# Kernel optimization log

Hardware: AMD Instinct MI355X
Metric: run time of the kernel (lower is better)

Reference implementation:

```python
import jax, jax.numpy as jnp
import numpy as np

N_PEGS = 32      # 33 holes, one empty at start
N_ACTIONS = 132  # 33 positions * 4 moves


def _constants():
    # English peg-solitaire board: 7x7 cross, 33 holes; hole 0 is the center (3,3).
    moves = np.array([[-1, 0], [1, 0], [0, -1], [0, 1]], dtype=np.int64)
    cells = [(i, j) for i in range(7) for j in range(7) if (2 <= i <= 4) or (2 <= j <= 4)]
    cells.remove((3, 3))
    grid = np.array([(3, 3)] + cells, dtype=np.int64)          # (33, 2)
    p2i = {tuple(p): k for k, p in enumerate(grid)}
    pos_ids = np.repeat(np.arange(33), 4)                      # (132,)
    move_ids = np.tile(np.arange(4), 33)                       # (132,)
    apos = grid[pos_ids]                                       # (132, 2)
    amov = moves[move_ids]
    midp = apos + amov
    tgtp = apos + 2 * amov
    mid_idx = np.array([p2i.get(tuple(p), 0) for p in midp], dtype=np.int64)
    tgt_idx = np.array([p2i.get(tuple(p), 0) for p in tgtp], dtype=np.int64)
    oob = np.array([(tuple(m) not in p2i) or (tuple(t) not in p2i)
                    for m, t in zip(midp, tgtp)], dtype=bool)  # (132,)
    return dict(
        action_pos_ids=jnp.asarray(pos_ids, dtype=jnp.int32),
        action_mid_indices=jnp.asarray(mid_idx, dtype=jnp.int32),
        action_target_indices=jnp.asarray(tgt_idx, dtype=jnp.int32),
        oob_mask=jnp.asarray(oob),
        i_indices=jnp.asarray(grid[:, 0], dtype=jnp.int32),
        j_indices=jnp.asarray(grid[:, 1], dtype=jnp.int32),
    )


def setup_inputs() -> dict:
    key = jax.random.key(0)
    n = 262144
    k1, k2, k3, k4 = jax.random.split(key, 4)
    pegs = (jax.random.uniform(k1, (n, 33)) > 0.5).astype(jnp.float32)
    n_pegs = jax.random.randint(k2, (n,), 2, 32).astype(jnp.int32)
    done = jnp.zeros((n,), dtype=bool)
    total_reward = jax.random.uniform(k3, (n,), dtype=jnp.float32)
    actions = jax.random.randint(k4, (n,), 0, N_ACTIONS).astype(jnp.int32)
    inp = {"pegs": pegs, "n_pegs": n_pegs, "done": done,
           "total_reward": total_reward, "actions": actions}
    inp.update(_constants())
    return inp


def _feasible(pegs, done, action_pos_ids, action_mid_indices,
              action_target_indices, oob_mask):
    # (n, 132) boolean feasible-action mask
    mask = ~oob_mask[None, :]
    no_peg = pegs == 0.0
    mask = mask & ~no_peg[:, action_pos_ids]          # source must have a peg
    mask = mask & (pegs[:, action_mid_indices] > 0)   # mid must have a peg
    mask = mask & (pegs[:, action_target_indices] == 0)  # target must be empty
    return mask & ~done[:, None]


def reference(pegs, n_pegs, done, total_reward, actions,
              action_pos_ids, action_mid_indices, action_target_indices,
              oob_mask, i_indices, j_indices):
    n = pegs.shape[0]
    env = jnp.arange(n)
    pos = action_pos_ids[actions]
    mid = action_mid_indices[actions]
    tgt = action_target_indices[actions]
    # execute the jump (same write order as torch: pos<-0, mid<-0, target<-1)
    pegs = pegs.at[env, pos].set(0.0).at[env, mid].set(0.0).at[env, tgt].set(1.0)
    n_pegs = n_pegs - 1
    rewards = jnp.where(n_pegs == 1, 1.0, 1.0 / (N_PEGS - 1)).astype(jnp.float32)
    done_win = n_pegs == 1
    feasible = _feasible(pegs, done, action_pos_ids, action_mid_indices,
                         action_target_indices, oob_mask)
    done_new = done_win | ~feasible.any(axis=1)
    total_reward = total_reward + rewards
    # state: (n, 7, 7, 3)
    ch0 = jnp.zeros((n, 7, 7), dtype=pegs.dtype).at[:, i_indices, j_indices].set(pegs)
    npf = n_pegs.astype(jnp.float32)
    peg_ratio = (npf - 1.0) / (N_PEGS - 1)
    removed_ratio = (N_PEGS - npf) / (N_PEGS - 1)
    states = jnp.stack([
        ch0,
        jnp.broadcast_to(peg_ratio[:, None, None], (n, 7, 7)),
        jnp.broadcast_to(removed_ratio[:, None, None], (n, 7, 7)),
    ], axis=-1)
    return rewards, states, done_new, pegs, n_pegs, total_reward
```

## Files before the change

### kernel.cpp

```cpp
#include <hip/hip_runtime.h>


#define EPB 256
#define NTH 256

typedef float f32x4 __attribute__((ext_vector_type(4)));

__device__ constexpr int C2B[33] = {
    24,  2,  3,  4,  9, 10, 11, 14, 15, 16, 17, 18, 19, 20,
    21, 22, 23, 25, 26, 27, 28, 29, 30, 31, 32, 33, 34,
    37, 38, 39, 44, 45, 46};

constexpr unsigned long long cross_mask() {
    unsigned long long b = 0;
    for (int i = 0; i < 7; ++i)
        for (int j = 0; j < 7; ++j)
            if ((i >= 2 && i <= 4) || (j >= 2 && j <= 4))
                b |= 1ull << (i * 7 + j);
    return b;
}
constexpr unsigned long long cols_le(int jmax) {
    unsigned long long b = 0;
    for (int i = 0; i < 7; ++i)
        for (int j = 0; j <= jmax; ++j) b |= 1ull << (i * 7 + j);
    return b;
}
constexpr unsigned long long cols_ge(int jmin) {
    unsigned long long b = 0;
    for (int i = 0; i < 7; ++i)
        for (int j = jmin; j < 7; ++j) b |= 1ull << (i * 7 + j);
    return b;
}
constexpr unsigned long long B_MASK = cross_mask();
constexpr unsigned long long C_LE4  = cols_le(4);
constexpr unsigned long long C_GE2  = cols_ge(2);

__global__ __launch_bounds__(NTH) void peg_step(
    const float* __restrict__ pegs_in,
    const int* __restrict__ n_pegs_in,
    const unsigned char* __restrict__ done_in,
    const float* __restrict__ tot_rew_in,
    const int* __restrict__ actions,
    const int* __restrict__ pos_ids,
    const int* __restrict__ mid_idx,
    const int* __restrict__ tgt_idx,
    const int* __restrict__ i_ind,
    const int* __restrict__ j_ind,
    float* __restrict__ out,
    int n)
{
    __shared__ int s_pos[132], s_mid[132], s_tgt[132];
    __shared__ int s_c2b[33];
    __shared__ unsigned long long s_bb[EPB];
    __shared__ float s_r1[EPB], s_r2[EPB];

    const int t  = threadIdx.x;
    const int e0 = blockIdx.x * EPB;
    const int e  = e0 + t;

    float* pegs_out = out + (size_t)149 * n;
    {
        const f32x4* src = (const f32x4*)(pegs_in + (size_t)e0 * 33);
        f32x4* dst = (f32x4*)(pegs_out + (size_t)e0 * 33);
        #pragma unroll
        for (int i = t; i < EPB * 33 / 4; i += NTH) dst[i] = src[i];
    }

    float rowv[33];
    {
        const float* row = pegs_in + (size_t)e * 33;
        #pragma unroll
        for (int c = 0; c < 33; ++c) rowv[c] = row[c];
    }

    const int a         = actions[e];
    const int np_new    = n_pegs_in[e] - 1;
    const bool done_old = (done_in[e] != 0);
    const float tot     = tot_rew_in[e];

    if (t < 132) { s_pos[t] = pos_ids[t]; s_mid[t] = mid_idx[t]; s_tgt[t] = tgt_idx[t]; }
    if (t < 33)  s_c2b[t] = i_ind[t] * 7 + j_ind[t];

    const float rw  = (np_new == 1) ? 1.0f : (1.0f / 31.0f);
    const float npf = (float)np_new;
    out[e]                   = rw;
    out[(size_t)182 * n + e] = npf;
    out[(size_t)183 * n + e] = tot + rw;

    __syncthreads();

    unsigned long long P = 0;
    #pragma unroll
    for (int c = 0; c < 33; ++c)
        P |= (unsigned long long)(rowv[c] != 0.0f) << C2B[c];

    const int p = s_pos[a], m = s_mid[a], g = s_tgt[a];
    const int bp = s_c2b[p], bm = s_c2b[m], bg = s_c2b[g];
    P &= ~(1ull << bp);
    P &= ~(1ull << bm);
    P |=  (1ull << bg);

    {
        float* od = pegs_out + (size_t)e * 33;
        od[p] = 0.0f;
        od[m] = 0.0f;
        od[g] = 1.0f;
    }

    const unsigned long long E = ~P & B_MASK;
    const unsigned long long feas =
        (P & (P >> 1) & (E >> 2)  & C_LE4) |
        (P & (P << 1) & (E << 2)  & C_GE2) |
        (P & (P >> 7) & (E >> 14))         |
        (P & (P << 7) & (E << 14));

    const bool dn = (np_new == 1) | done_old | (feas == 0ull);
    out[(size_t)148 * n + e] = dn ? 1.0f : 0.0f;

    s_bb[t] = P;
    s_r1[t] = (npf - 1.0f)  * (1.0f / 31.0f);
    s_r2[t] = (32.0f - npf) * (1.0f / 31.0f);
    __syncthreads();

    {
        f32x4* dst = (f32x4*)(out + (size_t)n + (size_t)e0 * 147);
        const int total = EPB * 147 / 4;
        for (int q = t; q < total; q += NTH) {
            const int f4  = q * 4;
            int env = f4 / 147;
            const int el = f4 - env * 147;
            int rc  = el / 3;
            int ch  = el - rc * 3;
            unsigned long long bb = s_bb[env];
            float r1 = s_r1[env], r2 = s_r2[env];
            f32x4 v;
            #pragma unroll
            for (int r = 0; r < 4; ++r) {
                v[r] = (ch == 0) ? (float)((unsigned int)(bb >> rc) & 1u)
                                 : ((ch == 1) ? r1 : r2);
                if (++ch == 3) {
                    ch = 0;
                    if (++rc == 49) {
                        rc = 0; ++env;
                        bb = s_bb[env]; r1 = s_r1[env]; r2 = s_r2[env];
                    }
                }
            }
            dst[q] = v;
        }
    }
}

extern "C" void kernel_launch(void* const* d_in, const int* in_sizes, int n_in,
                              void* d_out, int out_size, void* d_ws, size_t ws_size,
                              hipStream_t stream) {
    const float* pegs          = (const float*)d_in[0];
    const int* n_pegs          = (const int*)d_in[1];
    const unsigned char* done  = (const unsigned char*)d_in[2];
    const float* total_reward  = (const float*)d_in[3];
    const int* actions         = (const int*)d_in[4];
    const int* pos_ids         = (const int*)d_in[5];
    const int* mid_idx         = (const int*)d_in[6];
    const int* tgt_idx         = (const int*)d_in[7];
    const int* i_ind           = (const int*)d_in[9];
    const int* j_ind           = (const int*)d_in[10];
    float* out = (float*)d_out;

    int n = in_sizes[1];
    dim3 grid(n / EPB), block(NTH);
    hipLaunchKernelGGL(peg_step, grid, block, 0, stream,
                       pegs, n_pegs, done, total_reward, actions,
                       pos_ids, mid_idx, tgt_idx, i_ind, j_ind, out, n);
}
```

Measured before the change: 50.84 us.

## Stage peg rows through per-wave LDS and replace block barriers with wave fences

Each wave now copies its 64 environments' peg rows into shared memory with coalesced vector loads. It then reads each row from LDS, applies the jump there, and writes the whole tile out coalesced. This replaces the old approach of a direct global-to-global copy plus strided per-thread row reads and scattered global stores. The lookup tables are read directly from global memory instead of being staged in LDS, and the block-wide __syncthreads calls become wave-local waitcnt fences. This relies on cross-lane LDS visibility within a wave after lgkmcnt(0), and it uses more LDS per block, which may lower occupancy.

```diff
diff --git a/kernel.cpp b/kernel.cpp
--- a/kernel.cpp
+++ b/kernel.cpp
@@ -1,8 +1,9 @@
 #include <hip/hip_runtime.h>
 
 
-#define EPB 256
 #define NTH 256
+#define WPB 4
+#define EPW 64
 
 typedef float f32x4 __attribute__((ext_vector_type(4)));
 
@@ -35,6 +36,11 @@
 constexpr unsigned long long C_LE4  = cols_le(4);
 constexpr unsigned long long C_GE2  = cols_ge(2);
 
+__device__ __forceinline__ void wave_lds_fence() {
+    asm volatile("s_waitcnt lgkmcnt(0)" ::: "memory");
+    __builtin_amdgcn_sched_barrier(0);
+}
+
 __global__ __launch_bounds__(NTH) void peg_step(
     const float* __restrict__ pegs_in,
     const int* __restrict__ n_pegs_in,
@@ -49,37 +55,31 @@
     float* __restrict__ out,
     int n)
 {
-    __shared__ int s_pos[132], s_mid[132], s_tgt[132];
-    __shared__ int s_c2b[33];
-    __shared__ unsigned long long s_bb[EPB];
-    __shared__ float s_r1[EPB], s_r2[EPB];
+    __shared__ __align__(16) float s_pegs[WPB][EPW * 33];
+    __shared__ unsigned long long s_bb[WPB][EPW];
+    __shared__ float s_r1[WPB][EPW], s_r2[WPB][EPW];
 
-    const int t  = threadIdx.x;
-    const int e0 = blockIdx.x * EPB;
-    const int e  = e0 + t;
+    const int t    = threadIdx.x;
+    const int w    = t >> 6;
+    const int lane = t & 63;
+    const int ew0  = blockIdx.x * (WPB * EPW) + w * EPW;
+    const int e    = ew0 + lane;
 
-    float* pegs_out = out + (size_t)149 * n;
     {
-        const f32x4* src = (const f32x4*)(pegs_in + (size_t)e0 * 33);
-        f32x4* dst = (f32x4*)(pegs_out + (size_t)e0 * 33);
+        const f32x4* src = (const f32x4*)(pegs_in + (size_t)ew0 * 33);
+        f32x4* dst = (f32x4*)s_pegs[w];
         #pragma unroll
-        for (int i = t; i < EPB * 33 / 4; i += NTH) dst[i] = src[i];
-    }
-
-    float rowv[33];
-    {
-        const float* row = pegs_in + (size_t)e * 33;
-        #pragma unroll
-        for (int c = 0; c < 33; ++c) rowv[c] = row[c];
+        for (int i = lane; i < EPW * 33 / 4; i += 64) dst[i] = src[i];
     }
 
     const int a         = actions[e];
     const int np_new    = n_pegs_in[e] - 1;
     const bool done_old = (done_in[e] != 0);
     const float tot     = tot_rew_in[e];
-
-    if (t < 132) { s_pos[t] = pos_ids[t]; s_mid[t] = mid_idx[t]; s_tgt[t] = tgt_idx[t]; }
-    if (t < 33)  s_c2b[t] = i_ind[t] * 7 + j_ind[t];
+    const int p = pos_ids[a], m = mid_idx[a], g = tgt_idx[a];
+    const int bp = i_ind[p] * 7 + j_ind[p];
+    const int bm = i_ind[m] * 7 + j_ind[m];
+    const int bg = i_ind[g] * 7 + j_ind[g];
 
     const float rw  = (np_new == 1) ? 1.0f : (1.0f / 31.0f);
     const float npf = (float)np_new;
@@ -87,25 +87,20 @@
     out[(size_t)182 * n + e] = npf;
     out[(size_t)183 * n + e] = tot + rw;
 
-    __syncthreads();
+    wave_lds_fence();
 
+    float* row = s_pegs[w] + lane * 33;
     unsigned long long P = 0;
     #pragma unroll
     for (int c = 0; c < 33; ++c)
-        P |= (unsigned long long)(rowv[c] != 0.0f) << C2B[c];
+        P |= (unsigned long long)(row[c] != 0.0f) << C2B[c];
 
-    const int p = s_pos[a], m = s_mid[a], g = s_tgt[a];
-    const int bp = s_c2b[p], bm = s_c2b[m], bg = s_c2b[g];
+    row[p] = 0.0f;
+    row[m] = 0.0f;
+    row[g] = 1.0f;
     P &= ~(1ull << bp);
     P &= ~(1ull << bm);
     P |=  (1ull << bg);
-
-    {
-        float* od = pegs_out + (size_t)e * 33;
-        od[p] = 0.0f;
-        od[m] = 0.0f;
-        od[g] = 1.0f;
-    }
 
     const unsigned long long E = ~P & B_MASK;
     const unsigned long long feas =
@@ -117,34 +112,40 @@
     const bool dn = (np_new == 1) | done_old | (feas == 0ull);
     out[(size_t)148 * n + e] = dn ? 1.0f : 0.0f;
 
-    s_bb[t] = P;
-    s_r1[t] = (npf - 1.0f)  * (1.0f / 31.0f);
-    s_r2[t] = (32.0f - npf) * (1.0f / 31.0f);
-    __syncthreads();
+    s_bb[w][lane] = P;
+    s_r1[w][lane] = (npf - 1.0f)  * (1.0f / 31.0f);
+    s_r2[w][lane] = (32.0f - npf) * (1.0f / 31.0f);
+
+    wave_lds_fence();
 
     {
-        f32x4* dst = (f32x4*)(out + (size_t)n + (size_t)e0 * 147);
-        const int total = EPB * 147 / 4;
-        for (int q = t; q < total; q += NTH) {
-            const int f4  = q * 4;
+        const f32x4* src = (const f32x4*)s_pegs[w];
+        f32x4* dst = (f32x4*)(out + (size_t)149 * n + (size_t)ew0 * 33);
+        #pragma unroll
+        for (int i = lane; i < EPW * 33 / 4; i += 64) dst[i] = src[i];
+    }
+
+    {
+        f32x4* dst = (f32x4*)(out + (size_t)n + (size_t)ew0 * 147);
+        const int total = EPW * 147 / 4;
+        for (int q = lane; q < total; q += 64) {
+            const int f4 = q * 4;
             int env = f4 / 147;
-            const int el = f4 - env * 147;
-            int rc  = el / 3;
-            int ch  = el - rc * 3;
-            unsigned long long bb = s_bb[env];
-            float r1 = s_r1[env], r2 = s_r2[env];
+            int el  = f4 - env * 147;
+            unsigned long long bb = s_bb[w][env];
+            float r1 = s_r1[w][env], r2 = s_r2[w][env];
             f32x4 v;
             #pragma unroll
             for (int r = 0; r < 4; ++r) {
+                if (el == 147) {
+                    el = 0; ++env;
+                    bb = s_bb[w][env]; r1 = s_r1[w][env]; r2 = s_r2[w][env];
+                }
+                const int rc = el / 3;
+                const int ch = el - rc * 3;
                 v[r] = (ch == 0) ? (float)((unsigned int)(bb >> rc) & 1u)
                                  : ((ch == 1) ? r1 : r2);
-                if (++ch == 3) {
-                    ch = 0;
-                    if (++rc == 49) {
-                        rc = 0; ++env;
-                        bb = s_bb[env]; r1 = s_r1[env]; r2 = s_r2[env];
-                    }
-                }
+                ++el;
             }
             dst[q] = v;
         }
@@ -167,7 +168,7 @@
     float* out = (float*)d_out;
 
     int n = in_sizes[1];
-    dim3 grid(n / EPB), block(NTH);
+    dim3 grid(n / (WPB * EPW)), block(NTH);
     hipLaunchKernelGGL(peg_step, grid, block, 0, stream,
                        pegs, n_pegs, done, total_reward, actions,
                        pos_ids, mid_idx, tgt_idx, i_ind, j_ind, out, n);
```

Result: faster. 44.66 us (median of 2 runs) (-12.2%).
